# Kernel optimization log

Measured on AMD Instinct MI355X. Metric: run time of the kernel, lower is better.

The kernel has to match this reference:

```python
import jax, jax.numpy as jnp
import numpy as np

EPS = 8.0 / 255.0  # hparams['epsilon']


def setup_inputs() -> dict:
    key = jax.random.key(0)
    k1, k2, k3, k4 = jax.random.split(key, 4)
    B, N, C, H, Wd, K = 128, 96, 3, 32, 32, 10
    D = C * H * Wd
    imgs = jax.random.uniform(k1, (B, C, H, Wd), dtype=jnp.float32)
    # sample_deltas: uniform in [-eps, eps]
    deltas = 2.0 * EPS * jax.random.uniform(k2, (N, B, C, H, Wd), dtype=jnp.float32) - EPS
    W = jax.random.normal(k3, (D, K), dtype=jnp.float32) * (1.0 / np.sqrt(D))
    b = jnp.zeros((K,), dtype=jnp.float32)
    labels = jax.random.randint(k4, (B,), 0, K, dtype=jnp.int32)
    ind = 91  # math.ceil(N * proportion) - 1 with N=96, proportion=0.95
    return {"imgs": imgs, "deltas": deltas, "W": W, "b": b, "labels": labels, "ind": ind}


def reference(imgs, deltas, W, b, labels, ind):
    N, B = deltas.shape[:2]
    # pert_imgs = clamp(imgs + delta, 0, 1), flattened for the linear classifier
    x = jnp.clip(imgs[None] + deltas, 0.0, 1.0).reshape(N, B, -1)  # [N,B,D]
    logits = jnp.einsum('nbd,dk->nbk', x, W) + b                    # [N,B,K]
    logp = jax.nn.log_softmax(logits, axis=-1)
    # pert_loss1 = CE(logits, labels), per-sample
    loss1 = -jnp.take_along_axis(logp, labels[None, :, None], axis=-1)[..., 0]  # [N,B]
    # top-2 labels; new_labels = second-best class
    _, top2 = jax.lax.top_k(logits, 2)
    top1, second = top2[..., 0], top2[..., 1]
    loss2 = -jnp.take_along_axis(logp, second[..., None], axis=-1)[..., 0]      # [N,B]
    # mask: if argmax != label, pert_loss2[i] = -10000
    loss2 = jnp.where(top1 == labels[None, :], loss2, jnp.float32(-10000.0))
    # layout [B,N] as in torch.cat(..., dim=1)
    l1 = loss1.T
    l2 = loss2.T
    order = jnp.argsort(l1 - l2, axis=1)                 # sort(loss1 - loss2) indices
    sel_idx = order[:, ind]                              # per-sample selected column
    # torch.tensor(list) detaches -> no gradient through selected losses
    selected = jax.lax.stop_gradient(jnp.take_along_axis(l2, sel_idx[:, None], axis=1))  # [B,1]
    robust_loss = jnp.mean(jnp.mean(l1 - selected, axis=1))
    return robust_loss
```

## Files before the change

### kernel.cpp

```cpp
#include <hip/hip_runtime.h>
#include <math.h>

#define BB 128
#define NN 96
#define DD 3072
#define KK 10
#define G  4

__global__ __launch_bounds__(256) void k1_logits(
    const float* __restrict__ imgs,
    const float* __restrict__ deltas,
    const float* __restrict__ W,
    const float* __restrict__ bias,
    const int*   __restrict__ labels,
    float* __restrict__ l1_ws,
    float* __restrict__ l2_ws)
{
    const int t   = threadIdx.x;
    const int bid = blockIdx.x;
    const int b   = bid & 127;
    const int n0  = (bid >> 7) * G;

    float acc[G][KK];
#pragma unroll
    for (int j = 0; j < G; ++j)
#pragma unroll
        for (int k = 0; k < KK; ++k) acc[j][k] = 0.f;

#pragma unroll
    for (int c = 0; c < 3; ++c) {
        const int i0 = c * 1024 + t * 4;
        float w[40];
        const float4* wp = (const float4*)(W + (size_t)i0 * KK);
#pragma unroll
        for (int m = 0; m < 10; ++m) {
            float4 v = wp[m];
            w[4*m+0] = v.x; w[4*m+1] = v.y; w[4*m+2] = v.z; w[4*m+3] = v.w;
        }
        const float4 im = *(const float4*)(imgs + (size_t)b * DD + i0);
#pragma unroll
        for (int j = 0; j < G; ++j) {
            const int n = n0 + j;
            const float4 dl = *(const float4*)(deltas + ((size_t)(n * BB + b)) * DD + i0);
            const float x0 = fminf(fmaxf(im.x + dl.x, 0.f), 1.f);
            const float x1 = fminf(fmaxf(im.y + dl.y, 0.f), 1.f);
            const float x2 = fminf(fmaxf(im.z + dl.z, 0.f), 1.f);
            const float x3 = fminf(fmaxf(im.w + dl.w, 0.f), 1.f);
#pragma unroll
            for (int k = 0; k < KK; ++k) {
                acc[j][k] = fmaf(x3, w[30+k],
                            fmaf(x2, w[20+k],
                            fmaf(x1, w[10+k],
                            fmaf(x0, w[k], acc[j][k]))));
            }
        }
    }

    __shared__ float red[40 * 256];
#pragma unroll
    for (int j = 0; j < G; ++j)
#pragma unroll
        for (int k = 0; k < KK; ++k)
            red[(j * KK + k) * 256 + t] = acc[j][k];
    __syncthreads();

    const int wid  = t >> 6;
    const int lane = t & 63;
    float lg[KK];
#pragma unroll
    for (int k = 0; k < KK; ++k) {
        const float* row = red + (wid * KK + k) * 256;
        float s = row[lane] + row[lane + 64] + row[lane + 128] + row[lane + 192];
#pragma unroll
        for (int off = 32; off >= 1; off >>= 1)
            s += __shfl_down(s, off, 64);
        lg[k] = s;
    }

    if (lane == 0) {
        const int n = n0 + wid;
#pragma unroll
        for (int k = 0; k < KK; ++k) lg[k] += bias[k];
        int top1 = 0; float m1 = lg[0];
#pragma unroll
        for (int k = 1; k < KK; ++k) if (lg[k] > m1) { m1 = lg[k]; top1 = k; }
        int sec = (top1 == 0) ? 1 : 0; float m2 = lg[sec];
#pragma unroll
        for (int k = 0; k < KK; ++k)
            if (k != top1 && lg[k] > m2) { m2 = lg[k]; sec = k; }
        float se = 0.f;
#pragma unroll
        for (int k = 0; k < KK; ++k) se += expf(lg[k] - m1);
        const float lse = m1 + logf(se);
        const int lab = labels[b];
        const float loss1 = lse - lg[lab];
        const float loss2 = (top1 == lab) ? (lse - lg[sec]) : -10000.0f;
        l1_ws[b * NN + n] = loss1;
        l2_ws[b * NN + n] = loss2;
    }
}

__global__ __launch_bounds__(128) void k2_select(
    const float* __restrict__ l1_ws, const float* __restrict__ l2_ws,
    const int* __restrict__ ind_p, float* __restrict__ perb)
{
    const int b = blockIdx.x;
    const int t = threadIdx.x;
    __shared__ float sd[NN];
    __shared__ float sl2[NN];
    __shared__ float ssel;
    __shared__ float swsum[2];

    float myl1 = 0.f, myd = 0.f;
    if (t < NN) {
        const float a = l1_ws[b * NN + t];
        const float c = l2_ws[b * NN + t];
        myl1 = a; myd = a - c;
        sd[t] = myd; sl2[t] = c;
    }
    __syncthreads();

    if (t < NN) {
        int rank = 0;
        for (int j = 0; j < NN; ++j) {
            const float dj = sd[j];
            rank += (dj < myd) || (dj == myd && j < t);
        }
        if (rank == ind_p[0]) ssel = sl2[t];
    }

    float s = myl1;
#pragma unroll
    for (int off = 32; off >= 1; off >>= 1) s += __shfl_down(s, off, 64);
    if ((t & 63) == 0) swsum[t >> 6] = s;
    __syncthreads();
    if (t == 0) {
        const float total = swsum[0] + swsum[1];
        perb[b] = total / 96.0f - ssel;
    }
}

__global__ __launch_bounds__(128) void k3_final(
    const float* __restrict__ perb, float* __restrict__ out)
{
    const int t = threadIdx.x;
    float s = perb[t];
#pragma unroll
    for (int off = 32; off >= 1; off >>= 1) s += __shfl_down(s, off, 64);
    __shared__ float sw[2];
    if ((t & 63) == 0) sw[t >> 6] = s;
    __syncthreads();
    if (t == 0) out[0] = (sw[0] + sw[1]) / 128.0f;
}

extern "C" void kernel_launch(void* const* d_in, const int* in_sizes, int n_in,
                              void* d_out, int out_size, void* d_ws, size_t ws_size,
                              hipStream_t stream) {
    const float* imgs   = (const float*)d_in[0];
    const float* deltas = (const float*)d_in[1];
    const float* W      = (const float*)d_in[2];
    const float* bias   = (const float*)d_in[3];
    const int*   labels = (const int*)d_in[4];
    const int*   ind    = (const int*)d_in[5];
    float* out = (float*)d_out;

    float* l1_ws = (float*)d_ws;
    float* l2_ws = l1_ws + NN * BB;
    float* perb  = l2_ws + NN * BB;

    k1_logits<<<dim3(BB * (NN / G)), dim3(256), 0, stream>>>(
        imgs, deltas, W, bias, labels, l1_ws, l2_ws);
    k2_select<<<dim3(BB), dim3(128), 0, stream>>>(l1_ws, l2_ws, ind, perb);
    k3_final<<<dim3(1), dim3(128), 0, stream>>>(perb, out);
}
```

Baseline: 259.2 us.

## Assign one wavefront per (sample, noise-group) task and reduce logits with shuffles

Each wavefront now handles a whole (b, 4-noise) task and loops over the 3072-wide dot product in 12 chunks, instead of a 256-thread block sharing one task. The block-level shared-memory reduction and its __syncthreads are replaced by xor-shuffle butterfly reductions within the wave. The grid shrinks to 768 blocks, so there are fewer blocks, each doing more serial work per thread with a rolled loop. That may lower memory-level parallelism per task, and the 40 full butterflies add shuffle instructions.

```diff
diff --git a/kernel.cpp b/kernel.cpp
--- a/kernel.cpp
+++ b/kernel.cpp
@@ -16,10 +16,10 @@
     float* __restrict__ l1_ws,
     float* __restrict__ l2_ws)
 {
-    const int t   = threadIdx.x;
-    const int bid = blockIdx.x;
-    const int b   = bid & 127;
-    const int n0  = (bid >> 7) * G;
+    const int lane = threadIdx.x & 63;
+    const int task = blockIdx.x * 4 + (threadIdx.x >> 6);
+    const int b    = task & 127;
+    const int n0   = (task >> 7) * G;
 
     float acc[G][KK];
 #pragma unroll
@@ -27,9 +27,8 @@
 #pragma unroll
         for (int k = 0; k < KK; ++k) acc[j][k] = 0.f;
 
-#pragma unroll
-    for (int c = 0; c < 3; ++c) {
-        const int i0 = c * 1024 + t * 4;
+    for (int c = 0; c < 12; ++c) {
+        const int i0 = c * 256 + lane * 4;
         float w[40];
         const float4* wp = (const float4*)(W + (size_t)i0 * KK);
 #pragma unroll
@@ -56,31 +55,28 @@
         }
     }
 
-    __shared__ float red[40 * 256];
 #pragma unroll
     for (int j = 0; j < G; ++j)
 #pragma unroll
-        for (int k = 0; k < KK; ++k)
-            red[(j * KK + k) * 256 + t] = acc[j][k];
-    __syncthreads();
+        for (int k = 0; k < KK; ++k) {
+            float s = acc[j][k];
+#pragma unroll
+            for (int off = 1; off < 64; off <<= 1)
+                s += __shfl_xor(s, off, 64);
+            acc[j][k] = s;
+        }
 
-    const int wid  = t >> 6;
-    const int lane = t & 63;
-    float lg[KK];
+    if (lane < G) {
+        float lg[KK];
 #pragma unroll
-    for (int k = 0; k < KK; ++k) {
-        const float* row = red + (wid * KK + k) * 256;
-        float s = row[lane] + row[lane + 64] + row[lane + 128] + row[lane + 192];
-#pragma unroll
-        for (int off = 32; off >= 1; off >>= 1)
-            s += __shfl_down(s, off, 64);
-        lg[k] = s;
-    }
-
-    if (lane == 0) {
-        const int n = n0 + wid;
-#pragma unroll
-        for (int k = 0; k < KK; ++k) lg[k] += bias[k];
+        for (int k = 0; k < KK; ++k) {
+            float v = acc[0][k];
+            if (lane == 1) v = acc[1][k];
+            if (lane == 2) v = acc[2][k];
+            if (lane == 3) v = acc[3][k];
+            lg[k] = v + bias[k];
+        }
+        const int n = n0 + lane;
         int top1 = 0; float m1 = lg[0];
 #pragma unroll
         for (int k = 1; k < KK; ++k) if (lg[k] > m1) { m1 = lg[k]; top1 = k; }
@@ -168,7 +164,7 @@
     float* l2_ws = l1_ws + NN * BB;
     float* perb  = l2_ws + NN * BB;
 
-    k1_logits<<<dim3(BB * (NN / G)), dim3(256), 0, stream>>>(
+    k1_logits<<<dim3(768), dim3(256), 0, stream>>>(
         imgs, deltas, W, bias, labels, l1_ws, l2_ws);
     k2_select<<<dim3(BB), dim3(128), 0, stream>>>(l1_ws, l2_ws, ind, perb);
     k3_final<<<dim3(1), dim3(128), 0, stream>>>(perb, out);
```

Result: slower. 265.2 us (+2.3%).

## Halve k1 shared reduction via xor shuffle; merge select and final kernels

Applied to the files above, without the earlier changes.

In the logits kernel, adjacent lanes are pre-summed with an xor shuffle so only half the threads write partial sums, which halves the shared reduction buffer and the number of reads. The per-sample select kernel and the final mean kernel are merged into a single 1024-thread block. That block stages all losses in shared memory, ranks every entry, and reduces straight to the output. This removes one launch, but all the ranking work now runs on a single CU.

```diff
diff --git a/kernel.cpp b/kernel.cpp
--- a/kernel.cpp
+++ b/kernel.cpp
@@ -56,12 +56,22 @@
         }
     }
 
-    __shared__ float red[40 * 256];
+    __shared__ float red[40 * 128];
 #pragma unroll
     for (int j = 0; j < G; ++j)
 #pragma unroll
-        for (int k = 0; k < KK; ++k)
-            red[(j * KK + k) * 256 + t] = acc[j][k];
+        for (int k = 0; k < KK; ++k) {
+            float s = acc[j][k] + __shfl_xor(acc[j][k], 1, 64);
+            acc[j][k] = s;
+        }
+    if ((t & 1) == 0) {
+        const int col = t >> 1;
+#pragma unroll
+        for (int j = 0; j < G; ++j)
+#pragma unroll
+            for (int k = 0; k < KK; ++k)
+                red[(j * KK + k) * 128 + col] = acc[j][k];
+    }
     __syncthreads();
 
     const int wid  = t >> 6;
@@ -69,8 +79,8 @@
     float lg[KK];
 #pragma unroll
     for (int k = 0; k < KK; ++k) {
-        const float* row = red + (wid * KK + k) * 256;
-        float s = row[lane] + row[lane + 64] + row[lane + 128] + row[lane + 192];
+        const float* row = red + (wid * KK + k) * 128;
+        float s = row[lane] + row[lane + 64];
 #pragma unroll
         for (int off = 32; off >= 1; off >>= 1)
             s += __shfl_down(s, off, 64);
@@ -100,57 +110,58 @@
     }
 }
 
-__global__ __launch_bounds__(128) void k2_select(
+__global__ __launch_bounds__(1024) void k2_final(
     const float* __restrict__ l1_ws, const float* __restrict__ l2_ws,
-    const int* __restrict__ ind_p, float* __restrict__ perb)
+    const int* __restrict__ ind_p, float* __restrict__ out)
 {
-    const int b = blockIdx.x;
     const int t = threadIdx.x;
-    __shared__ float sd[NN];
-    __shared__ float sl2[NN];
-    __shared__ float ssel;
-    __shared__ float swsum[2];
+    __shared__ float sdiff[BB * NN];
+    __shared__ float sl2[BB * NN];
+    __shared__ float ssel[BB];
+    __shared__ float wpart[16];
 
-    float myl1 = 0.f, myd = 0.f;
-    if (t < NN) {
-        const float a = l1_ws[b * NN + t];
-        const float c = l2_ws[b * NN + t];
-        myl1 = a; myd = a - c;
-        sd[t] = myd; sl2[t] = c;
+    float suml1 = 0.f;
+#pragma unroll
+    for (int r = 0; r < 12; ++r) {
+        const int p = t + r * 1024;
+        const float a = l1_ws[p];
+        const float c = l2_ws[p];
+        suml1 += a;
+        sdiff[p] = a - c;
+        sl2[p]   = c;
     }
     __syncthreads();
 
-    if (t < NN) {
+    const int ind = ind_p[0];
+#pragma unroll
+    for (int r = 0; r < 12; ++r) {
+        const int p = t + r * 1024;
+        const int b = p / NN;
+        const int n = p - b * NN;
+        const float d = sdiff[p];
         int rank = 0;
+        const float* row = sdiff + b * NN;
         for (int j = 0; j < NN; ++j) {
-            const float dj = sd[j];
-            rank += (dj < myd) || (dj == myd && j < t);
+            const float dj = row[j];
+            rank += (dj < d) || (dj == d && j < n);
         }
-        if (rank == ind_p[0]) ssel = sl2[t];
+        if (rank == ind) ssel[b] = sl2[p];
     }
 
-    float s = myl1;
 #pragma unroll
-    for (int off = 32; off >= 1; off >>= 1) s += __shfl_down(s, off, 64);
-    if ((t & 63) == 0) swsum[t >> 6] = s;
+    for (int off = 32; off >= 1; off >>= 1) suml1 += __shfl_down(suml1, off, 64);
+    if ((t & 63) == 0) wpart[t >> 6] = suml1;
     __syncthreads();
-    if (t == 0) {
-        const float total = swsum[0] + swsum[1];
-        perb[b] = total / 96.0f - ssel;
+    if (t < 64) {
+        float s  = (t < 16) ? wpart[t] : 0.f;
+#pragma unroll
+        for (int off = 8; off >= 1; off >>= 1) s += __shfl_down(s, off, 64);
+        float se = ssel[t] + ssel[t + 64];
+#pragma unroll
+        for (int off = 32; off >= 1; off >>= 1) se += __shfl_down(se, off, 64);
+        if (t == 0)
+            out[0] = s / (96.0f * 128.0f) - se / 128.0f;
     }
-}
-
-__global__ __launch_bounds__(128) void k3_final(
-    const float* __restrict__ perb, float* __restrict__ out)
-{
-    const int t = threadIdx.x;
-    float s = perb[t];
-#pragma unroll
-    for (int off = 32; off >= 1; off >>= 1) s += __shfl_down(s, off, 64);
-    __shared__ float sw[2];
-    if ((t & 63) == 0) sw[t >> 6] = s;
-    __syncthreads();
-    if (t == 0) out[0] = (sw[0] + sw[1]) / 128.0f;
 }
 
 extern "C" void kernel_launch(void* const* d_in, const int* in_sizes, int n_in,
@@ -166,10 +177,8 @@
 
     float* l1_ws = (float*)d_ws;
     float* l2_ws = l1_ws + NN * BB;
-    float* perb  = l2_ws + NN * BB;
 
     k1_logits<<<dim3(BB * (NN / G)), dim3(256), 0, stream>>>(
         imgs, deltas, W, bias, labels, l1_ws, l2_ws);
-    k2_select<<<dim3(BB), dim3(128), 0, stream>>>(l1_ws, l2_ws, ind, perb);
-    k3_final<<<dim3(1), dim3(128), 0, stream>>>(perb, out);
+    k2_final<<<dim3(1), dim3(1024), 0, stream>>>(l1_ws, l2_ws, ind, out);
 }
```

Measured after the change: 318.6 us. 22.9% more time.
